# Kernel tuning notes

Hardware: AMD Instinct MI355X
Metric: run time of the kernel (lower is better)

Reference implementation:

```python
import jax, jax.numpy as jnp
import numpy as np

EPSILON = 1e-7  # wl-coref utils.add_dummy epsilon
LEAKY_SLOPE = 0.01  # torch.nn.LeakyReLU default

N_MENTIONS = 10000
BATCH = 512
N_ANTS = 50
MENTION_EMB = 1024
PW_EMB = 64
IN_FEATURES = 3 * MENTION_EMB + PW_EMB  # 3136
HIDDEN = 128


def setup_inputs() -> dict:
    key = jax.random.key(0)
    ks = jax.random.split(key, 9)
    return {
        "all_mentions": jax.random.normal(ks[0], (N_MENTIONS, MENTION_EMB), jnp.float32),
        "mentions_batch": jax.random.normal(ks[1], (BATCH, MENTION_EMB), jnp.float32),
        "pw_batch": jax.random.normal(ks[2], (BATCH, N_ANTS, PW_EMB), jnp.float32),
        "top_indices_batch": jax.random.randint(ks[3], (BATCH, N_ANTS), 0, N_MENTIONS, jnp.int64 if jax.config.jax_enable_x64 else jnp.int32),
        "top_rough_scores_batch": jax.random.normal(ks[4], (BATCH, N_ANTS), jnp.float32),
        "W1": jax.random.normal(ks[5], (IN_FEATURES, HIDDEN), jnp.float32) * 0.02,
        "b1": jax.random.normal(ks[6], (HIDDEN,), jnp.float32) * 0.02,
        "W_out": jax.random.normal(ks[7], (HIDDEN, 1), jnp.float32) * 0.02,
        "b_out": jax.random.normal(ks[8], (1,), jnp.float32) * 0.02,
    }


def reference(all_mentions, mentions_batch, pw_batch, top_indices_batch,
              top_rough_scores_batch, W1, b1, W_out, b_out):
    batch, n_ants = top_indices_batch.shape
    emb = mentions_batch.shape[1]
    # pair matrix: [batch, n_ants, 3*emb + pw_emb]
    a_mentions = jnp.broadcast_to(mentions_batch[:, None, :], (batch, n_ants, emb))
    b_mentions = all_mentions[top_indices_batch]          # gather: [batch, n_ants, emb]
    similarity = a_mentions * b_mentions
    pair_matrix = jnp.concatenate((a_mentions, b_mentions, similarity, pw_batch), axis=2)
    # FFNN: Linear -> LeakyReLU -> (Dropout=identity in eval) -> Linear(out=1)
    h = jax.nn.leaky_relu(jnp.einsum('baf,fh->bah', pair_matrix, W1) + b1, LEAKY_SLOPE)
    ffnn = (jnp.einsum('bah,ho->bao', h, W_out) + b_out)[..., 0]  # [batch, n_ants]
    scores = top_rough_scores_batch + ffnn
    # add_dummy(eps=True): prepend a column of EPSILON
    dummy = jnp.full((batch, 1), EPSILON, dtype=scores.dtype)
    return jnp.concatenate((dummy, scores), axis=1)  # [batch, n_ants + 1]
```

## Files before the change

kernel.cpp:

```cpp
#include <hip/hip_runtime.h>

#define N_MENT   10000
#define BATCH    512
#define N_ANTS   50
#define EMB      1024
#define PW_EMB   64
#define IN_F     3136
#define HID      128
#define M_TOT    (BATCH * N_ANTS)
#define EPS_VAL  1e-7f
#define SLOPE    0.01f

#define NKT      98
#define CONV_BLK 196
#define MAIN_BLK (M_TOT / 64)

using f32x4 = __attribute__((ext_vector_type(4))) float;
using s16x8 = __attribute__((ext_vector_type(8))) short;
using u16x4 = __attribute__((ext_vector_type(4))) unsigned short;
using u16x8 = __attribute__((ext_vector_type(8))) unsigned short;

__device__ __forceinline__ unsigned short f2bf(float f) {
  unsigned u = __builtin_bit_cast(unsigned, f);
  u += 0x7FFFu + ((u >> 16) & 1u);
  return (unsigned short)(u >> 16);
}

__device__ __forceinline__ u16x4 pack4(float4 v) {
  union { u16x4 o; unsigned u[2]; } r;
  asm("v_cvt_pk_bf16_f32 %0, %1, %2" : "=v"(r.u[0]) : "v"(v.x), "v"(v.y));
  asm("v_cvt_pk_bf16_f32 %0, %1, %2" : "=v"(r.u[1]) : "v"(v.z), "v"(v.w));
  return r.o;
}

__device__ __forceinline__ float4 fmul4(float4 a, float4 b) {
  return make_float4(a.x * b.x, a.y * b.y, a.z * b.z, a.w * b.w);
}

__device__ __forceinline__ int tile_orig_k(int tk) {
  if (tk >= 96) return 3072 + (tk - 96) * 32;
  const int c = tk / 6, r = tk % 6;
  return (r >> 1) * 1024 + c * 64 + (r & 1) * 32;
}

__global__ __launch_bounds__(256) void k_convert(const float* __restrict__ w1,
                                                 unsigned short* __restrict__ w1f) {
  const int id   = blockIdx.x * 256 + threadIdx.x;
  const int lane = id & 63;
  const int tile = id >> 6;
  const int tk   = tile % NKT, tn = tile / NKT;
  const int n    = tn * 16 + (lane & 15);
  const int k    = tile_orig_k(tk) + (lane >> 4) * 8;
  u16x8 o;
  #pragma unroll
  for (int j = 0; j < 8; ++j) o[j] = f2bf(w1[(size_t)(k + j) * HID + n]);
  *(u16x8*)(w1f + (size_t)id * 8) = o;
}

__global__ __launch_bounds__(512) void k_main(
    const float* __restrict__ all_m, const float* __restrict__ men,
    const float* __restrict__ pw, const int* __restrict__ topi,
    const float* __restrict__ rough, const unsigned short* __restrict__ w1f,
    const float* __restrict__ b1, const float* __restrict__ wout,
    const float* __restrict__ bout, float* __restrict__ out) {
  __shared__ __align__(16) unsigned short Xs[2][3][64 * 72];
  __shared__ float red[8][64];

  const int t  = threadIdx.x;
  const int m0 = blockIdx.x * 64;

  const int sr = t >> 3, sq = t & 7;
  const int m  = m0 + sr;
  const int bb = m / N_ANTS;
  const int bidx = topi[m];
  const float* pA = men   + (size_t)bb   * EMB    + sq * 8;
  const float* pB = all_m + (size_t)bidx * EMB    + sq * 8;
  const float* pP = pw    + (size_t)m    * PW_EMB + sq * 8;

  const int lane = t & 63, wid = t >> 6;
  const int ln = lane & 15, lg = lane >> 4;
  const unsigned short* wf = w1f + (size_t)wid * NKT * 512 + lane * 8;

  f32x4 acc[4] = {};

  float4 av0 = ((const float4*)pA)[0], av1 = ((const float4*)pA)[1];
  float4 bv0 = ((const float4*)pB)[0], bv1 = ((const float4*)pB)[1];

  s16x8 wcur[6], wnext[6];
  #pragma unroll
  for (int j = 0; j < 6; ++j)
    wcur[j] = *(const s16x8*)(wf + (size_t)j * 512);

  int buf = 0;
  for (int c = 0; c < 16; ++c) {
    *(u16x4*)&Xs[buf][0][sr * 72 + sq * 8]     = pack4(av0);
    *(u16x4*)&Xs[buf][0][sr * 72 + sq * 8 + 4] = pack4(av1);
    *(u16x4*)&Xs[buf][1][sr * 72 + sq * 8]     = pack4(bv0);
    *(u16x4*)&Xs[buf][1][sr * 72 + sq * 8 + 4] = pack4(bv1);
    *(u16x4*)&Xs[buf][2][sr * 72 + sq * 8]     = pack4(fmul4(av0, bv0));
    *(u16x4*)&Xs[buf][2][sr * 72 + sq * 8 + 4] = pack4(fmul4(av1, bv1));

    if (c < 15) {
      const float* qA = pA + (c + 1) * 64;
      const float* qB = pB + (c + 1) * 64;
      av0 = ((const float4*)qA)[0]; av1 = ((const float4*)qA)[1];
      bv0 = ((const float4*)qB)[0]; bv1 = ((const float4*)qB)[1];
    } else {
      av0 = ((const float4*)pP)[0]; av1 = ((const float4*)pP)[1];
    }

    #pragma unroll
    for (int j = 0; j < 6; ++j) {
      const int tkn = (c < 15) ? (c + 1) * 6 + j : (j < 2 ? 96 + j : 97);
      wnext[j] = *(const s16x8*)(wf + (size_t)tkn * 512);
    }

    __syncthreads();
    #pragma unroll
    for (int j = 0; j < 6; ++j) {
      const int reg = j >> 1, ks = j & 1;
      #pragma unroll
      for (int mt = 0; mt < 4; ++mt) {
        s16x8 x = *(const s16x8*)&Xs[buf][reg][(mt * 16 + ln) * 72 + ks * 32 + lg * 8];
        acc[mt] = __builtin_amdgcn_mfma_f32_16x16x32_bf16(x, wcur[j], acc[mt], 0, 0, 0);
      }
    }
    #pragma unroll
    for (int j = 0; j < 6; ++j) wcur[j] = wnext[j];
    buf ^= 1;
  }

  {
    *(u16x4*)&Xs[buf][0][sr * 72 + sq * 8]     = pack4(av0);
    *(u16x4*)&Xs[buf][0][sr * 72 + sq * 8 + 4] = pack4(av1);
    __syncthreads();
    #pragma unroll
    for (int ks = 0; ks < 2; ++ks)
      #pragma unroll
      for (int mt = 0; mt < 4; ++mt) {
        s16x8 x = *(const s16x8*)&Xs[buf][0][(mt * 16 + ln) * 72 + ks * 32 + lg * 8];
        acc[mt] = __builtin_amdgcn_mfma_f32_16x16x32_bf16(x, wcur[ks], acc[mt], 0, 0, 0);
      }
  }

  const int n0 = wid * 16 + ln;
  const float bias = b1[n0], w_o = wout[n0];
  #pragma unroll
  for (int mt = 0; mt < 4; ++mt)
    #pragma unroll
    for (int e = 0; e < 4; ++e) {
      float h = acc[mt][e] + bias;
      h = h > 0.f ? h : SLOPE * h;
      float ss = h * w_o;
      ss += __shfl_xor(ss, 1);
      ss += __shfl_xor(ss, 2);
      ss += __shfl_xor(ss, 4);
      ss += __shfl_xor(ss, 8);
      if (ln == 0) red[wid][mt * 16 + lg * 4 + e] = ss;
    }
  __syncthreads();
  if (t < 64) {
    const int gm = m0 + t;
    float v = red[0][t];
    #pragma unroll
    for (int w = 1; w < 8; ++w) v += red[w][t];
    const int gb = gm / N_ANTS;
    const int ga = gm - gb * N_ANTS;
    out[(size_t)gb * (N_ANTS + 1) + 1 + ga] = rough[gm] + v + bout[0];
  }
  if (t == 0) {
    for (int g = m0 / N_ANTS; g <= (m0 + 63) / N_ANTS; ++g)
      out[(size_t)g * (N_ANTS + 1)] = EPS_VAL;
  }
}

__global__ void k_eps(float* __restrict__ out) {
  out[(size_t)threadIdx.x * (N_ANTS + 1)] = EPS_VAL;
}

__global__ __launch_bounds__(128) void k_fb(const float* __restrict__ all_m,
                                            const float* __restrict__ men,
                                            const float* __restrict__ pw,
                                            const int*   __restrict__ topi,
                                            const float* __restrict__ rough,
                                            const float* __restrict__ w1,
                                            const float* __restrict__ b1,
                                            const float* __restrict__ wout,
                                            const float* __restrict__ bout,
                                            float* __restrict__ out) {
  __shared__ float xs[IN_F];
  __shared__ float hred[HID];
  const int pair = blockIdx.x;
  const int t = threadIdx.x;
  const int bb = pair / N_ANTS;
  const int idx = topi[pair];
  const float* pA = men + (size_t)bb * EMB;
  const float* pB = all_m + (size_t)idx * EMB;
  for (int k = t; k < EMB; k += 128) {
    float a = pA[k], b = pB[k];
    xs[k] = a; xs[EMB + k] = b; xs[2 * EMB + k] = a * b;
  }
  if (t < PW_EMB) xs[3 * EMB + t] = pw[(size_t)pair * PW_EMB + t];
  __syncthreads();
  float acc = 0.f;
  for (int k = 0; k < IN_F; ++k) acc = fmaf(xs[k], w1[(size_t)k * HID + t], acc);
  acc += b1[t];
  acc = acc > 0.f ? acc : SLOPE * acc;
  hred[t] = acc * wout[t];
  __syncthreads();
  for (int off = 64; off > 0; off >>= 1) {
    if (t < off) hred[t] += hred[t + off];
    __syncthreads();
  }
  if (t == 0)
    out[(size_t)bb * (N_ANTS + 1) + 1 + (pair - bb * N_ANTS)] = rough[pair] + hred[0] + bout[0];
}

extern "C" void kernel_launch(void* const* d_in, const int* in_sizes, int n_in,
                              void* d_out, int out_size, void* d_ws, size_t ws_size,
                              hipStream_t stream) {
  const float* all_m = (const float*)d_in[0];
  const float* men   = (const float*)d_in[1];
  const float* pw    = (const float*)d_in[2];
  const int*   topi  = (const int*)  d_in[3];
  const float* rough = (const float*)d_in[4];
  const float* w1    = (const float*)d_in[5];
  const float* b1    = (const float*)d_in[6];
  const float* wout  = (const float*)d_in[7];
  const float* bout  = (const float*)d_in[8];
  float* out = (float*)d_out;

  const size_t W1F_BYTES = (size_t)HID * IN_F * sizeof(unsigned short);

  if (ws_size >= W1F_BYTES) {
    unsigned short* w1f = (unsigned short*)d_ws;
    k_convert<<<CONV_BLK, 256, 0, stream>>>(w1, w1f);
    k_main<<<MAIN_BLK, 512, 0, stream>>>(all_m, men, pw, topi, rough, w1f,
                                         b1, wout, bout, out);
  } else {
    k_eps<<<1, BATCH, 0, stream>>>(out);
    k_fb<<<M_TOT, 128, 0, stream>>>(all_m, men, pw, topi, rough, w1, b1, wout, bout, out);
  }
}
```

Baseline: 49.22 us.

## Switch to 32x32x16 bf16 MFMA with 2x4 warp tiling and swizzled LDS

Replaces the 16x16x32 MFMA tiles (each warp owning 16 hidden columns across all 64 rows) with 32x32x16 MFMA, where each warp owns a 32x32 output tile in a 2x4 warp grid. The weight pre-layout is rebuilt for 32-wide K=16 tiles. The padded LDS rows are replaced with an XOR swizzle so 16-byte writes and reads avoid bank conflicts. The change cuts LDS reads per MFMA and the cross-warp reduction width, at the cost of more weight registers per warp (12 prefetched fragments) and a 4-blocks-per-CU occupancy hint that may pressure registers.

```diff
diff --git a/kernel.cpp b/kernel.cpp
--- a/kernel.cpp
+++ b/kernel.cpp
@@ -11,14 +11,14 @@
 #define EPS_VAL  1e-7f
 #define SLOPE    0.01f
 
-#define NKT      98
+#define NKT      196
 #define CONV_BLK 196
 #define MAIN_BLK (M_TOT / 64)
 
-using f32x4 = __attribute__((ext_vector_type(4))) float;
-using s16x8 = __attribute__((ext_vector_type(8))) short;
-using u16x4 = __attribute__((ext_vector_type(4))) unsigned short;
-using u16x8 = __attribute__((ext_vector_type(8))) unsigned short;
+using f32x4  = __attribute__((ext_vector_type(4)))  float;
+using f32x16 = __attribute__((ext_vector_type(16))) float;
+using s16x8  = __attribute__((ext_vector_type(8)))  short;
+using u16x8  = __attribute__((ext_vector_type(8)))  unsigned short;
 
 __device__ __forceinline__ unsigned short f2bf(float f) {
   unsigned u = __builtin_bit_cast(unsigned, f);
@@ -26,11 +26,13 @@
   return (unsigned short)(u >> 16);
 }
 
-__device__ __forceinline__ u16x4 pack4(float4 v) {
-  union { u16x4 o; unsigned u[2]; } r;
-  asm("v_cvt_pk_bf16_f32 %0, %1, %2" : "=v"(r.u[0]) : "v"(v.x), "v"(v.y));
-  asm("v_cvt_pk_bf16_f32 %0, %1, %2" : "=v"(r.u[1]) : "v"(v.z), "v"(v.w));
-  return r.o;
+__device__ __forceinline__ u16x8 pack8(float4 lo, float4 hi) {
+  union { u16x8 v; unsigned u[4]; } r;
+  asm("v_cvt_pk_bf16_f32 %0, %1, %2" : "=v"(r.u[0]) : "v"(lo.x), "v"(lo.y));
+  asm("v_cvt_pk_bf16_f32 %0, %1, %2" : "=v"(r.u[1]) : "v"(lo.z), "v"(lo.w));
+  asm("v_cvt_pk_bf16_f32 %0, %1, %2" : "=v"(r.u[2]) : "v"(hi.x), "v"(hi.y));
+  asm("v_cvt_pk_bf16_f32 %0, %1, %2" : "=v"(r.u[3]) : "v"(hi.z), "v"(hi.w));
+  return r.v;
 }
 
 __device__ __forceinline__ float4 fmul4(float4 a, float4 b) {
@@ -38,9 +40,9 @@
 }
 
 __device__ __forceinline__ int tile_orig_k(int tk) {
-  if (tk >= 96) return 3072 + (tk - 96) * 32;
-  const int c = tk / 6, r = tk % 6;
-  return (r >> 1) * 1024 + c * 64 + (r & 1) * 32;
+  if (tk >= 192) return 3072 + (tk - 192) * 16;
+  const int c = tk / 12, r = tk % 12;
+  return (r >> 2) * 1024 + c * 64 + (r & 3) * 16;
 }
 
 __global__ __launch_bounds__(256) void k_convert(const float* __restrict__ w1,
@@ -49,22 +51,22 @@
   const int lane = id & 63;
   const int tile = id >> 6;
   const int tk   = tile % NKT, tn = tile / NKT;
-  const int n    = tn * 16 + (lane & 15);
-  const int k    = tile_orig_k(tk) + (lane >> 4) * 8;
+  const int n    = tn * 32 + (lane & 31);
+  const int k    = tile_orig_k(tk) + (lane >> 5) * 8;
   u16x8 o;
   #pragma unroll
   for (int j = 0; j < 8; ++j) o[j] = f2bf(w1[(size_t)(k + j) * HID + n]);
   *(u16x8*)(w1f + (size_t)id * 8) = o;
 }
 
-__global__ __launch_bounds__(512) void k_main(
+__global__ __launch_bounds__(512, 4) void k_main(
     const float* __restrict__ all_m, const float* __restrict__ men,
     const float* __restrict__ pw, const int* __restrict__ topi,
     const float* __restrict__ rough, const unsigned short* __restrict__ w1f,
     const float* __restrict__ b1, const float* __restrict__ wout,
     const float* __restrict__ bout, float* __restrict__ out) {
-  __shared__ __align__(16) unsigned short Xs[2][3][64 * 72];
-  __shared__ float red[8][64];
+  __shared__ __align__(16) unsigned short Xs[2][3][64 * 64];
+  __shared__ float red[4][64];
 
   const int t  = threadIdx.x;
   const int m0 = blockIdx.x * 64;
@@ -76,29 +78,34 @@
   const float* pA = men   + (size_t)bb   * EMB    + sq * 8;
   const float* pB = all_m + (size_t)bidx * EMB    + sq * 8;
   const float* pP = pw    + (size_t)m    * PW_EMB + sq * 8;
+  const int widx = sr * 64 + (((sq * 16) ^ ((sr & 7) << 4)) >> 1);
 
   const int lane = t & 63, wid = t >> 6;
-  const int ln = lane & 15, lg = lane >> 4;
-  const unsigned short* wf = w1f + (size_t)wid * NKT * 512 + lane * 8;
-
-  f32x4 acc[4] = {};
+  const int rowL = lane & 31, lh = lane >> 5;
+  const int tn = wid & 3, mt = wid >> 2;
+  const unsigned short* wf = w1f + (size_t)tn * NKT * 512 + lane * 8;
+
+  const int grow = mt * 32 + rowL;
+  int ridx[4];
+  #pragma unroll
+  for (int ks = 0; ks < 4; ++ks)
+    ridx[ks] = grow * 64 + ((((ks * 32 + lh * 16)) ^ ((grow & 7) << 4)) >> 1);
+
+  f32x16 acc = {};
 
   float4 av0 = ((const float4*)pA)[0], av1 = ((const float4*)pA)[1];
   float4 bv0 = ((const float4*)pB)[0], bv1 = ((const float4*)pB)[1];
 
-  s16x8 wcur[6], wnext[6];
-  #pragma unroll
-  for (int j = 0; j < 6; ++j)
+  s16x8 wcur[12], wnext[12];
+  #pragma unroll
+  for (int j = 0; j < 12; ++j)
     wcur[j] = *(const s16x8*)(wf + (size_t)j * 512);
 
   int buf = 0;
   for (int c = 0; c < 16; ++c) {
-    *(u16x4*)&Xs[buf][0][sr * 72 + sq * 8]     = pack4(av0);
-    *(u16x4*)&Xs[buf][0][sr * 72 + sq * 8 + 4] = pack4(av1);
-    *(u16x4*)&Xs[buf][1][sr * 72 + sq * 8]     = pack4(bv0);
-    *(u16x4*)&Xs[buf][1][sr * 72 + sq * 8 + 4] = pack4(bv1);
-    *(u16x4*)&Xs[buf][2][sr * 72 + sq * 8]     = pack4(fmul4(av0, bv0));
-    *(u16x4*)&Xs[buf][2][sr * 72 + sq * 8 + 4] = pack4(fmul4(av1, bv1));
+    *(u16x8*)&Xs[buf][0][widx] = pack8(av0, av1);
+    *(u16x8*)&Xs[buf][1][widx] = pack8(bv0, bv1);
+    *(u16x8*)&Xs[buf][2][widx] = pack8(fmul4(av0, bv0), fmul4(av1, bv1));
 
     if (c < 15) {
       const float* qA = pA + (c + 1) * 64;
@@ -110,60 +117,55 @@
     }
 
     #pragma unroll
-    for (int j = 0; j < 6; ++j) {
-      const int tkn = (c < 15) ? (c + 1) * 6 + j : (j < 2 ? 96 + j : 97);
+    for (int j = 0; j < 12; ++j) {
+      const int tkn = (c < 15) ? (c + 1) * 12 + j : 192 + (j & 3);
       wnext[j] = *(const s16x8*)(wf + (size_t)tkn * 512);
     }
 
     __syncthreads();
     #pragma unroll
-    for (int j = 0; j < 6; ++j) {
-      const int reg = j >> 1, ks = j & 1;
+    for (int reg = 0; reg < 3; ++reg)
       #pragma unroll
-      for (int mt = 0; mt < 4; ++mt) {
-        s16x8 x = *(const s16x8*)&Xs[buf][reg][(mt * 16 + ln) * 72 + ks * 32 + lg * 8];
-        acc[mt] = __builtin_amdgcn_mfma_f32_16x16x32_bf16(x, wcur[j], acc[mt], 0, 0, 0);
+      for (int ks = 0; ks < 4; ++ks) {
+        s16x8 x = *(const s16x8*)&Xs[buf][reg][ridx[ks]];
+        acc = __builtin_amdgcn_mfma_f32_32x32x16_bf16(x, wcur[reg * 4 + ks], acc, 0, 0, 0);
       }
-    }
-    #pragma unroll
-    for (int j = 0; j < 6; ++j) wcur[j] = wnext[j];
+    #pragma unroll
+    for (int j = 0; j < 12; ++j) wcur[j] = wnext[j];
     buf ^= 1;
   }
 
   {
-    *(u16x4*)&Xs[buf][0][sr * 72 + sq * 8]     = pack4(av0);
-    *(u16x4*)&Xs[buf][0][sr * 72 + sq * 8 + 4] = pack4(av1);
+    *(u16x8*)&Xs[buf][0][widx] = pack8(av0, av1);
     __syncthreads();
     #pragma unroll
-    for (int ks = 0; ks < 2; ++ks)
-      #pragma unroll
-      for (int mt = 0; mt < 4; ++mt) {
-        s16x8 x = *(const s16x8*)&Xs[buf][0][(mt * 16 + ln) * 72 + ks * 32 + lg * 8];
-        acc[mt] = __builtin_amdgcn_mfma_f32_16x16x32_bf16(x, wcur[ks], acc[mt], 0, 0, 0);
-      }
-  }
-
-  const int n0 = wid * 16 + ln;
+    for (int ks = 0; ks < 4; ++ks) {
+      s16x8 x = *(const s16x8*)&Xs[buf][0][ridx[ks]];
+      acc = __builtin_amdgcn_mfma_f32_32x32x16_bf16(x, wcur[ks], acc, 0, 0, 0);
+    }
+  }
+
+  const int n0 = tn * 32 + rowL;
   const float bias = b1[n0], w_o = wout[n0];
   #pragma unroll
-  for (int mt = 0; mt < 4; ++mt)
-    #pragma unroll
-    for (int e = 0; e < 4; ++e) {
-      float h = acc[mt][e] + bias;
-      h = h > 0.f ? h : SLOPE * h;
-      float ss = h * w_o;
-      ss += __shfl_xor(ss, 1);
-      ss += __shfl_xor(ss, 2);
-      ss += __shfl_xor(ss, 4);
-      ss += __shfl_xor(ss, 8);
-      if (ln == 0) red[wid][mt * 16 + lg * 4 + e] = ss;
-    }
+  for (int e = 0; e < 16; ++e) {
+    float h = acc[e] + bias;
+    h = h > 0.f ? h : SLOPE * h;
+    float ss = h * w_o;
+    ss += __shfl_xor(ss, 1);
+    ss += __shfl_xor(ss, 2);
+    ss += __shfl_xor(ss, 4);
+    ss += __shfl_xor(ss, 8);
+    ss += __shfl_xor(ss, 16);
+    if (rowL == 0) {
+      const int rl = (e & 3) + 8 * (e >> 2) + 4 * lh;
+      red[tn][mt * 32 + rl] = ss;
+    }
+  }
   __syncthreads();
   if (t < 64) {
     const int gm = m0 + t;
-    float v = red[0][t];
-    #pragma unroll
-    for (int w = 1; w < 8; ++w) v += red[w][t];
+    const float v = red[0][t] + red[1][t] + red[2][t] + red[3][t];
     const int gb = gm / N_ANTS;
     const int ga = gm - gb * N_ANTS;
     out[(size_t)gb * (N_ANTS + 1) + 1 + ga] = rough[gm] + v + bout[0];
```

New measurement: 117.4 us. 139% more time.
